# Kernel optimization log

Hardware: AMD Instinct MI355X
Metric: run time of the kernel (lower is better)

## Reference

```python
import jax, jax.numpy as jnp
import numpy as np

T, N, F_IN, H, C, E = 64, 2000, 32, 64, 10, 32000
EPS = 1e-5  # BatchNorm eps (PyG BatchNorm default)


def setup_inputs() -> dict:
    key = jax.random.key(0)
    ks = jax.random.split(key, 32)
    nrm = lambda i, shape, s=0.05: jax.random.normal(ks[i], shape, jnp.float32) * s
    return {
        "x_seq": jax.random.normal(ks[0], (T, N, F_IN), jnp.float32),
        "edge_index": jax.random.randint(ks[1], (2, E), 0, N),
        "edge_weight": jax.random.uniform(ks[2], (E,), jnp.float32),
        "causal_weight": nrm(3, (N, N), 0.01),  # torch.randn(N,N)*0.01
        "lin_in_w": nrm(4, (H, F_IN)), "lin_in_b": nrm(5, (H,)),
        "fusion_w": nrm(6, (H, 2 * H)), "fusion_b": nrm(7, (H,)),
        "gcn_w0": nrm(8, (H, H)), "gcn_b0": nrm(9, (H,)),
        "gcn_w1": nrm(10, (H, H)), "gcn_b1": nrm(11, (H,)),
        "bn0_g": jnp.ones((H,), jnp.float32), "bn0_b": jnp.zeros((H,), jnp.float32),
        "bn0_m": nrm(12, (H,)), "bn0_v": 0.5 + jax.random.uniform(ks[13], (H,), jnp.float32),
        "bn1_g": jnp.ones((H,), jnp.float32), "bn1_b": jnp.zeros((H,), jnp.float32),
        "bn1_m": nrm(14, (H,)), "bn1_v": 0.5 + jax.random.uniform(ks[15], (H,), jnp.float32),
        "gru_wih0": nrm(16, (3 * H, H)), "gru_whh0": nrm(17, (3 * H, H)),
        "gru_bih0": nrm(18, (3 * H,)), "gru_bhh0": nrm(19, (3 * H,)),
        "gru_wih1": nrm(20, (3 * H, H)), "gru_whh1": nrm(21, (3 * H, H)),
        "gru_bih1": nrm(22, (3 * H,)), "gru_bhh1": nrm(23, (3 * H,)),
        "bnout_g": jnp.ones((H,), jnp.float32), "bnout_b": jnp.zeros((H,), jnp.float32),
        "bnout_m": nrm(24, (H,)), "bnout_v": 0.5 + jax.random.uniform(ks[25], (H,), jnp.float32),
        "lin_out_w": nrm(26, (C, H)), "lin_out_b": nrm(27, (C,)),
    }


def _bn(x, g, b, m, v):
    # eval-mode BatchNorm over the feature (last) axis with running stats
    return (x - m) * jax.lax.rsqrt(v + EPS) * g + b


def _gru_layer(xs, wih, whh, bih, bhh):
    # torch nn.GRU single layer, batch_first=False: xs [T, B, H_in]
    n_batch, h = xs.shape[1], whh.shape[1]

    def step(hprev, xt):
        gi = xt @ wih.T + bih            # [B, 3H]
        gh = hprev @ whh.T + bhh         # [B, 3H]
        i_r, i_z, i_n = jnp.split(gi, 3, axis=-1)
        h_r, h_z, h_n = jnp.split(gh, 3, axis=-1)
        r = jax.nn.sigmoid(i_r + h_r)
        z = jax.nn.sigmoid(i_z + h_z)
        n = jnp.tanh(i_n + r * h_n)
        hnew = (1.0 - z) * n + z * hprev
        return hnew, hnew

    h0 = jnp.zeros((n_batch, h), xs.dtype)
    _, ys = jax.lax.scan(step, h0, xs)
    return ys


def reference(x_seq, edge_index, edge_weight, causal_weight, lin_in_w, lin_in_b,
              fusion_w, fusion_b, gcn_w0, gcn_b0, gcn_w1, gcn_b1,
              bn0_g, bn0_b, bn0_m, bn0_v, bn1_g, bn1_b, bn1_m, bn1_v,
              gru_wih0, gru_whh0, gru_bih0, gru_bhh0,
              gru_wih1, gru_whh1, gru_bih1, gru_bhh1,
              bnout_g, bnout_b, bnout_m, bnout_v, lin_out_w, lin_out_b):
    n = x_seq.shape[1]
    src, dst = edge_index[0], edge_index[1]
    loops = jnp.arange(n)
    # GCN normalization with added self-loops (PyG gcn_norm, fill_value=1)
    src_f = jnp.concatenate([src, loops])
    dst_f = jnp.concatenate([dst, loops])
    w_f = jnp.concatenate([edge_weight, jnp.ones((n,), edge_weight.dtype)])
    deg = jnp.zeros((n,), x_seq.dtype).at[dst_f].add(w_f)
    dis = jax.lax.rsqrt(jnp.maximum(deg, 1e-12))
    norm = dis[src_f] * w_f * dis[dst_f]             # [E+N]

    # per-timestep pipeline, vectorized over T (same math as the Python loop)
    x = jax.nn.relu(jnp.einsum('tnf,hf->tnh', x_seq, lin_in_w) + lin_in_b)  # [T,N,H]
    wc = jax.nn.softmax(causal_weight, axis=1)                              # [N,N]
    x_agg = jnp.einsum('ij,tjh->tih', wc, x)
    x = jax.nn.relu(jnp.concatenate([x, x_agg], axis=-1) @ fusion_w.T + fusion_b)

    def gcn(xx, w, b):
        xw = xx @ w.T                                         # [T,N,H]
        msgs = jnp.take(xw, src_f, axis=1) * norm[None, :, None]  # [T,E+N,H]
        agg = jnp.zeros_like(xw).at[:, dst_f].add(msgs)
        return agg + b

    x = jax.nn.relu(_bn(gcn(x, gcn_w0, gcn_b0), bn0_g, bn0_b, bn0_m, bn0_v))
    # dropout between GCN layers is identity in eval mode
    x = jax.nn.relu(_bn(gcn(x, gcn_w1, gcn_b1), bn1_g, bn1_b, bn1_m, bn1_v))

    h = _gru_layer(x, gru_wih0, gru_whh0, gru_bih0, gru_bhh0)
    h = _gru_layer(h, gru_wih1, gru_whh1, gru_bih1, gru_bhh1)
    h_last = jax.nn.relu(_bn(h[-1], bnout_g, bnout_b, bnout_m, bnout_v))
    out = h_last @ lin_out_w.T + lin_out_b                   # [N, C]
    return jax.nn.log_softmax(out, axis=-1)
```

## Files before the change

kernel.cpp:

```cpp
#include <hip/hip_runtime.h>
#include <hip/hip_bf16.h>
#include <math.h>

#define TT 64
#define NN 2000
#define FIN 32
#define HH 64
#define CC 10
#define EE 32000
#define ETOT 34000
#define THL 4096
#define EPSBN 1e-5f
#define NB 16

#define OFF_WC   0u
#define OFF_XA   4000000u
#define OFF_XB   12192000u
#define OFF_XC   20384000u
#define OFF_DEG  28576000u
#define OFF_H1   28578048u
#define OFF_CNT  28706048u
#define OFF_CUR  28708096u
#define OFF_OFF  28710144u
#define OFF_CSRS 28712208u
#define OFF_CSRN 28746224u
#define OFF_HST  28780240u

typedef __attribute__((ext_vector_type(8))) short short8v;
typedef __attribute__((ext_vector_type(4))) float f32x4;

__device__ __forceinline__ float fsigmoid(float x) { return 1.f / (1.f + __expf(-x)); }
__device__ __forceinline__ float ftanh(float x) {
    float e = __expf(2.f * x);
    return (e - 1.f) / (e + 1.f);
}
__device__ __forceinline__ unsigned short f2bf(float f) {
    __hip_bfloat16 h = __float2bfloat16(f);
    return *reinterpret_cast<unsigned short*>(&h);
}
__device__ __forceinline__ float bf2f(unsigned short u) {
    unsigned int x = ((unsigned int)u) << 16;
    return __int_as_float(x);
}
__device__ __forceinline__ void gload_lds16(const unsigned short* g, unsigned short* l) {
    __builtin_amdgcn_global_load_lds(
        (const __attribute__((address_space(1))) unsigned int*)g,
        (__attribute__((address_space(3))) unsigned int*)l,
        16, 0, 0);
}

__global__ void k_zero(int* cnt, int* cur, float* deg) {
    int i = blockIdx.x * 256 + threadIdx.x;
    if (i < 2048) { cnt[i] = 0; cur[i] = 0; deg[i] = 0.f; }
}

__global__ void k_count(const int* __restrict__ ei, const float* __restrict__ ew,
                        int* cnt, float* deg) {
    int e = blockIdx.x * 256 + threadIdx.x;
    if (e < ETOT) {
        int dst; float w;
        if (e < EE) { dst = ei[EE + e]; w = ew[e]; }
        else        { dst = e - EE;     w = 1.f; }
        atomicAdd(&cnt[dst], 1);
        atomicAdd(&deg[dst], w);
    }
}

__global__ __launch_bounds__(1024) void k_scan(const int* __restrict__ cnt, int* off) {
    __shared__ int s[2048];
    int tid = threadIdx.x;
    s[tid]        = (tid        < NN) ? cnt[tid]        : 0;
    s[tid + 1024] = (tid + 1024 < NN) ? cnt[tid + 1024] : 0;
    __syncthreads();
    for (int d = 1; d < 2048; d <<= 1) {
        int idx = (tid + 1) * (d << 1) - 1;
        if (idx < 2048) s[idx] += s[idx - d];
        __syncthreads();
    }
    if (tid == 0) s[2047] = 0;
    __syncthreads();
    for (int d = 1024; d >= 1; d >>= 1) {
        int idx = (tid + 1) * (d << 1) - 1;
        if (idx < 2048) { int t = s[idx - d]; s[idx - d] = s[idx]; s[idx] += t; }
        __syncthreads();
    }
    off[tid] = s[tid];
    off[tid + 1024] = s[tid + 1024];
}

__global__ void k_fill(const int* __restrict__ ei, const float* __restrict__ ew,
                       const float* __restrict__ deg, const int* __restrict__ off,
                       int* cur, int* csr_src, float* csr_nrm) {
    int e = blockIdx.x * 256 + threadIdx.x;
    if (e < ETOT) {
        int src, dst; float w;
        if (e < EE) { src = ei[e]; dst = ei[EE + e]; w = ew[e]; }
        else        { src = dst = e - EE;            w = 1.f; }
        float ds = rsqrtf(fmaxf(deg[src], 1e-12f));
        float dd = rsqrtf(fmaxf(deg[dst], 1e-12f));
        int pos = off[dst] + atomicAdd(&cur[dst], 1);
        csr_src[pos] = src;
        csr_nrm[pos] = ds * w * dd;
    }
}

__global__ __launch_bounds__(256) void k_softmax(const float* __restrict__ CW,
                                                 unsigned short* __restrict__ WCH) {
    __shared__ float row[NN];
    __shared__ float red[256];
    int r = blockIdx.x, tid = threadIdx.x;
    const float* in = CW + (size_t)r * NN;
    float mx = -1e30f;
    for (int i = tid; i < NN; i += 256) { float v = in[i]; row[i] = v; mx = fmaxf(mx, v); }
    red[tid] = mx; __syncthreads();
    for (int s = 128; s > 0; s >>= 1) {
        if (tid < s) red[tid] = fmaxf(red[tid], red[tid + s]);
        __syncthreads();
    }
    mx = red[0]; __syncthreads();
    float sm = 0.f;
    for (int i = tid; i < NN; i += 256) { float e = __expf(row[i] - mx); row[i] = e; sm += e; }
    red[tid] = sm; __syncthreads();
    for (int s = 128; s > 0; s >>= 1) {
        if (tid < s) red[tid] += red[tid + s];
        __syncthreads();
    }
    float inv = 1.f / red[0];
    unsigned short* out = WCH + (size_t)r * 2048;
    for (int i = tid; i < 2048; i += 256)
        out[i] = (i < NN) ? f2bf(row[i] * inv) : (unsigned short)0;
}

__global__ __launch_bounds__(256) void k_lin2(const float* __restrict__ XS,
                                              const float* __restrict__ W,
                                              const float* __restrict__ b,
                                              unsigned short* __restrict__ OUT) {
    __shared__ float Wt[FIN][68];
    __shared__ float As[FIN][68];
    int tid = threadIdx.x;
    int n = blockIdx.x;
    for (int i = tid; i < HH * FIN; i += 256) { int o = i >> 5, k = i & 31; Wt[k][o] = W[i]; }
    int row = tid >> 2, kq = tid & 3;
    {
        const float4* src = (const float4*)(XS + ((size_t)row * NN + n) * FIN + kq * 8);
        float4 v0 = src[0], v1 = src[1];
        As[kq * 8 + 0][row] = v0.x; As[kq * 8 + 1][row] = v0.y;
        As[kq * 8 + 2][row] = v0.z; As[kq * 8 + 3][row] = v0.w;
        As[kq * 8 + 4][row] = v1.x; As[kq * 8 + 5][row] = v1.y;
        As[kq * 8 + 6][row] = v1.z; As[kq * 8 + 7][row] = v1.w;
    }
    __syncthreads();
    int tx = tid & 15, ty = tid >> 4;
    float acc[4][4] = {};
#pragma unroll
    for (int k = 0; k < FIN; ++k) {
        float4 av = *(const float4*)&As[k][ty * 4];
        float4 wv = *(const float4*)&Wt[k][tx * 4];
        acc[0][0] += av.x * wv.x; acc[0][1] += av.x * wv.y; acc[0][2] += av.x * wv.z; acc[0][3] += av.x * wv.w;
        acc[1][0] += av.y * wv.x; acc[1][1] += av.y * wv.y; acc[1][2] += av.y * wv.z; acc[1][3] += av.y * wv.w;
        acc[2][0] += av.z * wv.x; acc[2][1] += av.z * wv.y; acc[2][2] += av.z * wv.z; acc[2][3] += av.z * wv.w;
        acc[3][0] += av.w * wv.x; acc[3][1] += av.w * wv.y; acc[3][2] += av.w * wv.z; acc[3][3] += av.w * wv.w;
    }
    float4 bv = *(const float4*)(b + tx * 4);
#pragma unroll
    for (int ii = 0; ii < 4; ++ii) {
        float o0 = fmaxf(acc[ii][0] + bv.x, 0.f);
        float o1 = fmaxf(acc[ii][1] + bv.y, 0.f);
        float o2 = fmaxf(acc[ii][2] + bv.z, 0.f);
        float o3 = fmaxf(acc[ii][3] + bv.w, 0.f);
        unsigned int p0 = (unsigned int)f2bf(o0) | ((unsigned int)f2bf(o1) << 16);
        unsigned int p1 = (unsigned int)f2bf(o2) | ((unsigned int)f2bf(o3) << 16);
        uint2 pk; pk.x = p0; pk.y = p1;
        *(uint2*)(OUT + ((size_t)n * TT + ty * 4 + ii) * HH + tx * 4) = pk;
    }
}

__global__ __launch_bounds__(256) void k_tr(const unsigned short* __restrict__ X,
                                            unsigned short* __restrict__ XT) {
    __shared__ unsigned short tile[64][65];
    int cb = blockIdx.x * 64;
    int kb = blockIdx.y * 64;
    int tid = threadIdx.x;
    int r = tid >> 2, cq = tid & 3;
    unsigned short vals[16];
    if (kb + r < NN) {
        const uint4* src = (const uint4*)(X + (size_t)(kb + r) * THL + cb + cq * 16);
        uint4 u0 = src[0], u1 = src[1];
        *(uint4*)vals = u0; *(uint4*)(vals + 8) = u1;
    } else {
#pragma unroll
        for (int j = 0; j < 16; ++j) vals[j] = 0;
    }
#pragma unroll
    for (int j = 0; j < 16; ++j) tile[cq * 16 + j][r] = vals[j];
    __syncthreads();
    int cl = tid >> 2, kq = tid & 3;
    unsigned short tmp[16];
#pragma unroll
    for (int j = 0; j < 16; ++j) tmp[j] = tile[cl][kq * 16 + j];
    unsigned short* dst = XT + (size_t)(cb + cl) * 2048 + kb + kq * 16;
    *(uint4*)dst = *(uint4*)tmp;
    *(uint4*)(dst + 8) = *(uint4*)(tmp + 8);
}

__global__ __launch_bounds__(256, 1) void k_gemm_bf(const unsigned short* __restrict__ A,
                                                    const unsigned short* __restrict__ B,
                                                    unsigned short* __restrict__ CH) {
    __shared__ unsigned short As[128][64];
    __shared__ unsigned short Bs[128][64];
    int tid = threadIdx.x;
    int mb = blockIdx.y * 128, nb = blockIdx.x * 128;
    int w = tid >> 6, lane = tid & 63;
    int wr = w >> 1, wc = w & 1;
    int l15 = lane & 15, l4 = lane >> 4;
    f32x4 acc[4][4] = {};
    int r_base = w * 8 + (lane >> 3);
    int colu = (lane & 7) * 8;
    for (int kt = 0; kt < 32; ++kt) {
        __syncthreads();
#pragma unroll
        for (int c = 0; c < 4; ++c) {
            int row = c * 32 + r_base;
            gload_lds16(A + (size_t)(mb + row) * 2048 + kt * 64 + colu, &As[c * 32 + w * 8][0]);
            gload_lds16(B + (size_t)(nb + row) * 2048 + kt * 64 + colu, &Bs[c * 32 + w * 8][0]);
        }
        __syncthreads();
#pragma unroll
        for (int kk = 0; kk < 2; ++kk) {
            short8v af[4], bfr[4];
#pragma unroll
            for (int f = 0; f < 4; ++f) {
                af[f]  = *(const short8v*)&As[wr * 64 + f * 16 + l15][kk * 32 + l4 * 8];
                bfr[f] = *(const short8v*)&Bs[wc * 64 + f * 16 + l15][kk * 32 + l4 * 8];
            }
#pragma unroll
            for (int fm = 0; fm < 4; ++fm)
#pragma unroll
                for (int fn = 0; fn < 4; ++fn)
                    acc[fm][fn] = __builtin_amdgcn_mfma_f32_16x16x32_bf16(af[fm], bfr[fn], acc[fm][fn], 0, 0, 0);
        }
    }
    unsigned short* epi = (unsigned short*)(&As[0][0]) + (size_t)w * (16 * 72);
    int erow8 = lane >> 3;
    int ecol8 = lane & 7;
#pragma unroll
    for (int fm = 0; fm < 4; ++fm) {
        __syncthreads();
#pragma unroll
        for (int fn = 0; fn < 4; ++fn)
#pragma unroll
            for (int rr = 0; rr < 4; ++rr)
                epi[(l4 * 4 + rr) * 72 + fn * 16 + l15] = f2bf(acc[fm][fn][rr]);
        __syncthreads();
#pragma unroll
        for (int rh = 0; rh < 2; ++rh) {
            int lrow = rh * 8 + erow8;
            int grow = mb + wr * 64 + fm * 16 + lrow;
            if (grow < NN) {
                *(uint4*)(CH + (size_t)grow * THL + nb + wc * 64 + ecol8 * 8)
                    = *(const uint4*)&epi[lrow * 72 + ecol8 * 8];
            }
        }
    }
}

__global__ __launch_bounds__(256) void k_fusxw(const unsigned short* __restrict__ X,
                                               const unsigned short* __restrict__ XAH,
                                               const float* __restrict__ W,
                                               const float* __restrict__ b,
                                               const float* __restrict__ W0,
                                               unsigned short* __restrict__ OUT) {
    __shared__ float Wt[2 * HH][68];
    __shared__ float As[HH][68];
    int tid = threadIdx.x;
    size_t r0 = (size_t)blockIdx.x * 64;
    for (int i = tid; i < HH * 2 * HH; i += 256) { int o = i >> 7, k = i & 127; Wt[k][o] = W[i]; }
    int row = tid >> 2, kq = tid & 3;
    int tx = tid & 15, ty = tid >> 4;
    float acc[4][4] = {};
    __syncthreads();
    {
        const uint4* s = (const uint4*)(X + (r0 + row) * HH + kq * 16);
        uint4 u0 = s[0], u1 = s[1];
        unsigned short us[16];
        *(uint4*)us = u0; *(uint4*)(us + 8) = u1;
#pragma unroll
        for (int j = 0; j < 16; ++j)
            As[kq * 16 + j][row] = bf2f(us[j]);
    }
    __syncthreads();
#pragma unroll
    for (int k = 0; k < HH; ++k) {
        float4 av = *(const float4*)&As[k][ty * 4];
        float4 wv = *(const float4*)&Wt[k][tx * 4];
        acc[0][0] += av.x * wv.x; acc[0][1] += av.x * wv.y; acc[0][2] += av.x * wv.z; acc[0][3] += av.x * wv.w;
        acc[1][0] += av.y * wv.x; acc[1][1] += av.y * wv.y; acc[1][2] += av.y * wv.z; acc[1][3] += av.y * wv.w;
        acc[2][0] += av.z * wv.x; acc[2][1] += av.z * wv.y; acc[2][2] += av.z * wv.z; acc[2][3] += av.z * wv.w;
        acc[3][0] += av.w * wv.x; acc[3][1] += av.w * wv.y; acc[3][2] += av.w * wv.z; acc[3][3] += av.w * wv.w;
    }
    __syncthreads();
    {
        const uint4* s = (const uint4*)(XAH + (r0 + row) * HH + kq * 16);
        uint4 u0 = s[0], u1 = s[1];
        unsigned short us[16];
        *(uint4*)us = u0; *(uint4*)(us + 8) = u1;
#pragma unroll
        for (int j = 0; j < 16; ++j)
            As[kq * 16 + j][row] = bf2f(us[j]);
    }
    __syncthreads();
#pragma unroll
    for (int k = 0; k < HH; ++k) {
        float4 av = *(const float4*)&As[k][ty * 4];
        float4 wv = *(const float4*)&Wt[HH + k][tx * 4];
        acc[0][0] += av.x * wv.x; acc[0][1] += av.x * wv.y; acc[0][2] += av.x * wv.z; acc[0][3] += av.x * wv.w;
        acc[1][0] += av.y * wv.x; acc[1][1] += av.y * wv.y; acc[1][2] += av.y * wv.z; acc[1][3] += av.y * wv.w;
        acc[2][0] += av.z * wv.x; acc[2][1] += av.z * wv.y; acc[2][2] += av.z * wv.z; acc[2][3] += av.z * wv.w;
        acc[3][0] += av.w * wv.x; acc[3][1] += av.w * wv.y; acc[3][2] += av.w * wv.z; acc[3][3] += av.w * wv.w;
    }
    float4 bv = *(const float4*)(b + tx * 4);
    __syncthreads();
#pragma unroll
    for (int ii = 0; ii < 4; ++ii) {
        As[tx * 4 + 0][ty * 4 + ii] = fmaxf(acc[ii][0] + bv.x, 0.f);
        As[tx * 4 + 1][ty * 4 + ii] = fmaxf(acc[ii][1] + bv.y, 0.f);
        As[tx * 4 + 2][ty * 4 + ii] = fmaxf(acc[ii][2] + bv.z, 0.f);
        As[tx * 4 + 3][ty * 4 + ii] = fmaxf(acc[ii][3] + bv.w, 0.f);
    }
    for (int i = tid; i < HH * HH; i += 256) { int o = i >> 6, k = i & 63; Wt[k][o] = W0[i]; }
    __syncthreads();
    float a2[4][4] = {};
#pragma unroll
    for (int k = 0; k < HH; ++k) {
        float4 av = *(const float4*)&As[k][ty * 4];
        float4 wv = *(const float4*)&Wt[k][tx * 4];
        a2[0][0] += av.x * wv.x; a2[0][1] += av.x * wv.y; a2[0][2] += av.x * wv.z; a2[0][3] += av.x * wv.w;
        a2[1][0] += av.y * wv.x; a2[1][1] += av.y * wv.y; a2[1][2] += av.y * wv.z; a2[1][3] += av.y * wv.w;
        a2[2][0] += av.z * wv.x; a2[2][1] += av.z * wv.y; a2[2][2] += av.z * wv.z; a2[2][3] += av.z * wv.w;
        a2[3][0] += av.w * wv.x; a2[3][1] += av.w * wv.y; a2[3][2] += av.w * wv.z; a2[3][3] += av.w * wv.w;
    }
#pragma unroll
    for (int ii = 0; ii < 4; ++ii) {
        unsigned int p0 = (unsigned int)f2bf(a2[ii][0]) | ((unsigned int)f2bf(a2[ii][1]) << 16);
        unsigned int p1 = (unsigned int)f2bf(a2[ii][2]) | ((unsigned int)f2bf(a2[ii][3]) << 16);
        uint2 pk; pk.x = p0; pk.y = p1;
        *(uint2*)(OUT + (r0 + ty * 4 + ii) * HH + tx * 4) = pk;
    }
}

__global__ __launch_bounds__(256) void k_aggxw(const unsigned short* __restrict__ XW,
                                               const int* __restrict__ off,
                                               const int* __restrict__ csr_src,
                                               const float* __restrict__ csr_nrm,
                                               const float* __restrict__ bias,
                                               const float* __restrict__ g,
                                               const float* __restrict__ bb,
                                               const float* __restrict__ m,
                                               const float* __restrict__ v,
                                               const float* __restrict__ W1,
                                               unsigned short* __restrict__ OUT) {
    __shared__ float Rs[HH][18];
    __shared__ float Wt[HH][68];
    int dst = blockIdx.x, ch = blockIdx.y, tid = threadIdx.x;
    int base = ch * 1024 + tid * 4;
    for (int i = tid; i < HH * HH; i += 256) { int o = i >> 6, k = i & 63; Wt[k][o] = W1[i]; }
    float4 acc = make_float4(0.f, 0.f, 0.f, 0.f);
    int beg = off[dst], end = off[dst + 1];
    for (int e = beg; e < end; ++e) {
        int src = csr_src[e];
        float w = csr_nrm[e];
        uint2 u = *(const uint2*)(XW + (size_t)src * THL + base);
        acc.x += w * bf2f((unsigned short)(u.x & 0xffff));
        acc.y += w * bf2f((unsigned short)(u.x >> 16));
        acc.z += w * bf2f((unsigned short)(u.y & 0xffff));
        acc.w += w * bf2f((unsigned short)(u.y >> 16));
    }
    int h0 = base & 63;
    int rloc = tid >> 4;
    float4 bs = *(const float4*)(bias + h0);
    float4 gv = *(const float4*)(g + h0);
    float4 vv = *(const float4*)(v + h0);
    float4 mv = *(const float4*)(m + h0);
    float4 bv = *(const float4*)(bb + h0);
    Rs[h0 + 0][rloc] = fmaxf((acc.x + bs.x - mv.x) * rsqrtf(vv.x + EPSBN) * gv.x + bv.x, 0.f);
    Rs[h0 + 1][rloc] = fmaxf((acc.y + bs.y - mv.y) * rsqrtf(vv.y + EPSBN) * gv.y + bv.y, 0.f);
    Rs[h0 + 2][rloc] = fmaxf((acc.z + bs.z - mv.z) * rsqrtf(vv.z + EPSBN) * gv.z + bv.z, 0.f);
    Rs[h0 + 3][rloc] = fmaxf((acc.w + bs.w - mv.w) * rsqrtf(vv.w + EPSBN) * gv.w + bv.w, 0.f);
    __syncthreads();
    int c4 = tid & 15;
    float a2[4] = {0.f, 0.f, 0.f, 0.f};
#pragma unroll
    for (int k = 0; k < HH; ++k) {
        float a = Rs[k][rloc];
        float4 wv = *(const float4*)&Wt[k][c4 * 4];
        a2[0] += a * wv.x; a2[1] += a * wv.y; a2[2] += a * wv.z; a2[3] += a * wv.w;
    }
    size_t grow = (size_t)dst * TT + ch * 16 + rloc;
    unsigned int p0 = (unsigned int)f2bf(a2[0]) | ((unsigned int)f2bf(a2[1]) << 16);
    unsigned int p1 = (unsigned int)f2bf(a2[2]) | ((unsigned int)f2bf(a2[3]) << 16);
    uint2 pk; pk.x = p0; pk.y = p1;
    *(uint2*)(OUT + grow * HH + c4 * 4) = pk;
}

__global__ __launch_bounds__(256) void k_agg(const unsigned short* __restrict__ XW,
                                             const int* __restrict__ off,
                                             const int* __restrict__ csr_src,
                                             const float* __restrict__ csr_nrm,
                                             const float* __restrict__ bias,
                                             const float* __restrict__ g,
                                             const float* __restrict__ bb,
                                             const float* __restrict__ m,
                                             const float* __restrict__ v,
                                             unsigned short* __restrict__ OUT) {
    int dst = blockIdx.x, ch = blockIdx.y, tid = threadIdx.x;
    int base = ch * 1024 + tid * 4;
    float4 acc = make_float4(0.f, 0.f, 0.f, 0.f);
    int beg = off[dst], end = off[dst + 1];
    for (int e = beg; e < end; ++e) {
        int src = csr_src[e];
        float w = csr_nrm[e];
        uint2 u = *(const uint2*)(XW + (size_t)src * THL + base);
        acc.x += w * bf2f((unsigned short)(u.x & 0xffff));
        acc.y += w * bf2f((unsigned short)(u.x >> 16));
        acc.z += w * bf2f((unsigned short)(u.y & 0xffff));
        acc.w += w * bf2f((unsigned short)(u.y >> 16));
    }
    int h0 = base & 63;
    float4 bs = *(const float4*)(bias + h0);
    float4 gv = *(const float4*)(g + h0);
    float4 vv = *(const float4*)(v + h0);
    float4 mv = *(const float4*)(m + h0);
    float4 bv = *(const float4*)(bb + h0);
    float o0 = fmaxf((acc.x + bs.x - mv.x) * rsqrtf(vv.x + EPSBN) * gv.x + bv.x, 0.f);
    float o1 = fmaxf((acc.y + bs.y - mv.y) * rsqrtf(vv.y + EPSBN) * gv.y + bv.y, 0.f);
    float o2 = fmaxf((acc.z + bs.z - mv.z) * rsqrtf(vv.z + EPSBN) * gv.z + bv.z, 0.f);
    float o3 = fmaxf((acc.w + bs.w - mv.w) * rsqrtf(vv.w + EPSBN) * gv.w + bv.w, 0.f);
    unsigned int p0 = (unsigned int)f2bf(o0) | ((unsigned int)f2bf(o1) << 16);
    unsigned int p1 = (unsigned int)f2bf(o2) | ((unsigned int)f2bf(o3) << 16);
    uint2 pk; pk.x = p0; pk.y = p1;
    *(uint2*)(OUT + (size_t)dst * THL + base) = pk;
}

__global__ __launch_bounds__(256, 1) void k_gruM(const unsigned short* __restrict__ IN,
                                                 const float* __restrict__ wih0, const float* __restrict__ whh0,
                                                 const float* __restrict__ bih0, const float* __restrict__ bhh0,
                                                 const float* __restrict__ wih1, const float* __restrict__ whh1,
                                                 const float* __restrict__ bih1, const float* __restrict__ bhh1,
                                                 float* __restrict__ hout) {
    __shared__ float hf0[NB][68];
    __shared__ float hf1[NB][68];
    __shared__ unsigned short hb0[NB][72];
    __shared__ unsigned short hb1[NB][72];
    int tid = threadIdx.x;
    int w = tid >> 6, lane = tid & 63;
    int l15 = lane & 15, l4 = lane >> 4;
    int nb0 = blockIdx.x * NB;
    short8v bw[4][3][2];
    const float* Wm[4] = { wih0, whh0, wih1, whh1 };
#pragma unroll
    for (int m = 0; m < 4; ++m)
#pragma unroll
        for (int g = 0; g < 3; ++g)
#pragma unroll
            for (int kk = 0; kk < 2; ++kk) {
                const float* src = Wm[m] + (size_t)(64 * g + 16 * w + l15) * HH + kk * 32 + l4 * 8;
                float4 v0 = *(const float4*)src;
                float4 v1 = *(const float4*)(src + 4);
                short8v f;
                f[0] = (short)f2bf(v0.x); f[1] = (short)f2bf(v0.y);
                f[2] = (short)f2bf(v0.z); f[3] = (short)f2bf(v0.w);
                f[4] = (short)f2bf(v1.x); f[5] = (short)f2bf(v1.y);
                f[6] = (short)f2bf(v1.z); f[7] = (short)f2bf(v1.w);
                bw[m][g][kk] = f;
            }
    int jr = 16 * w + l15;
    float b0r = bih0[jr] + bhh0[jr];
    float b0z = bih0[64 + jr] + bhh0[64 + jr];
    float b0n = bih0[128 + jr];
    float h0n = bhh0[128 + jr];
    float b1r = bih1[jr] + bhh1[jr];
    float b1z = bih1[64 + jr] + bhh1[64 + jr];
    float b1n = bih1[128 + jr];
    float h1n = bhh1[128 + jr];
    for (int i = tid; i < NB * 68; i += 256) { ((float*)hf0)[i] = 0.f; ((float*)hf1)[i] = 0.f; }
    for (int i = tid; i < NB * 72; i += 256) { ((unsigned short*)hb0)[i] = 0; ((unsigned short*)hb1)[i] = 0; }
    __syncthreads();
    const unsigned short* xb = IN + (size_t)(nb0 + l15) * (TT * HH);
    uint4 xu[2];
    xu[0] = *(const uint4*)(xb + l4 * 8);
    xu[1] = *(const uint4*)(xb + 32 + l4 * 8);
#pragma unroll 1
    for (int t = 0; t <= TT; ++t) {
        bool act0 = (t < TT);
        bool act1 = (t >= 1);
        short8v ax[2], ah0[2], ah1[2];
        ax[0] = *(const short8v*)&xu[0];
        ax[1] = *(const short8v*)&xu[1];
#pragma unroll
        for (int kk = 0; kk < 2; ++kk) {
            ah0[kk] = *(const short8v*)&hb0[l15][kk * 32 + l4 * 8];
            ah1[kk] = *(const short8v*)&hb1[l15][kk * 32 + l4 * 8];
        }
        __syncthreads();
        if (t + 1 < TT) {
            const unsigned short* xs = xb + (size_t)(t + 1) * HH;
            xu[0] = *(const uint4*)(xs + l4 * 8);
            xu[1] = *(const uint4*)(xs + 32 + l4 * 8);
        }
        if (act0) {
            f32x4 gr = { b0r, b0r, b0r, b0r };
            f32x4 gz = { b0z, b0z, b0z, b0z };
            f32x4 gn = { b0n, b0n, b0n, b0n };
            f32x4 hr = { 0.f, 0.f, 0.f, 0.f };
            f32x4 hz = { 0.f, 0.f, 0.f, 0.f };
            f32x4 hn = { h0n, h0n, h0n, h0n };
#pragma unroll
            for (int kk = 0; kk < 2; ++kk) {
                gr = __builtin_amdgcn_mfma_f32_16x16x32_bf16(ax[kk], bw[0][0][kk], gr, 0, 0, 0);
                gz = __builtin_amdgcn_mfma_f32_16x16x32_bf16(ax[kk], bw[0][1][kk], gz, 0, 0, 0);
                gn = __builtin_amdgcn_mfma_f32_16x16x32_bf16(ax[kk], bw[0][2][kk], gn, 0, 0, 0);
                hr = __builtin_amdgcn_mfma_f32_16x16x32_bf16(ah0[kk], bw[1][0][kk], hr, 0, 0, 0);
                hz = __builtin_amdgcn_mfma_f32_16x16x32_bf16(ah0[kk], bw[1][1][kk], hz, 0, 0, 0);
                hn = __builtin_amdgcn_mfma_f32_16x16x32_bf16(ah0[kk], bw[1][2][kk], hn, 0, 0, 0);
            }
#pragma unroll
            for (int i = 0; i < 4; ++i) {
                int node = l4 * 4 + i;
                float r = fsigmoid(gr[i] + hr[i]);
                float z = fsigmoid(gz[i] + hz[i]);
                float nn2 = ftanh(gn[i] + r * hn[i]);
                float ho = hf0[node][jr];
                float hv = (1.f - z) * nn2 + z * ho;
                hf0[node][jr] = hv;
                hb0[node][jr] = f2bf(hv);
            }
        }
        if (act1) {
            f32x4 gr = { b1r, b1r, b1r, b1r };
            f32x4 gz = { b1z, b1z, b1z, b1z };
            f32x4 gn = { b1n, b1n, b1n, b1n };
            f32x4 hr = { 0.f, 0.f, 0.f, 0.f };
            f32x4 hz = { 0.f, 0.f, 0.f, 0.f };
            f32x4 hn = { h1n, h1n, h1n, h1n };
#pragma unroll
            for (int kk = 0; kk < 2; ++kk) {
                gr = __builtin_amdgcn_mfma_f32_16x16x32_bf16(ah0[kk], bw[2][0][kk], gr, 0, 0, 0);
                gz = __builtin_amdgcn_mfma_f32_16x16x32_bf16(ah0[kk], bw[2][1][kk], gz, 0, 0, 0);
                gn = __builtin_amdgcn_mfma_f32_16x16x32_bf16(ah0[kk], bw[2][2][kk], gn, 0, 0, 0);
                hr = __builtin_amdgcn_mfma_f32_16x16x32_bf16(ah1[kk], bw[3][0][kk], hr, 0, 0, 0);
                hz = __builtin_amdgcn_mfma_f32_16x16x32_bf16(ah1[kk], bw[3][1][kk], hz, 0, 0, 0);
                hn = __builtin_amdgcn_mfma_f32_16x16x32_bf16(ah1[kk], bw[3][2][kk], hn, 0, 0, 0);
            }
#pragma unroll
            for (int i = 0; i < 4; ++i) {
                int node = l4 * 4 + i;
                float r = fsigmoid(gr[i] + hr[i]);
                float z = fsigmoid(gz[i] + hz[i]);
                float nn2 = ftanh(gn[i] + r * hn[i]);
                float ho = hf1[node][jr];
                float hv = (1.f - z) * nn2 + z * ho;
                hf1[node][jr] = hv;
                hb1[node][jr] = f2bf(hv);
            }
        }
        __syncthreads();
    }
    for (int i = tid; i < NB * HH; i += 256) {
        int node = i >> 6, j = i & 63;
        hout[(size_t)(nb0 + node) * HH + j] = hf1[node][j];
    }
}

__global__ __launch_bounds__(256) void k_head(const float* __restrict__ Hf,
                                              const float* __restrict__ g, const float* __restrict__ b,
                                              const float* __restrict__ m, const float* __restrict__ v,
                                              const float* __restrict__ W, const float* __restrict__ wb,
                                              float* __restrict__ out) {
    __shared__ float hb[4][HH];
    __shared__ float lg[4][CC];
    int tid = threadIdx.x;
    int n0 = blockIdx.x * 4;
    int wv = tid >> 6, lane = tid & 63;
    int n = n0 + wv;
    float x = Hf[(size_t)n * HH + lane];
    x = (x - m[lane]) * rsqrtf(v[lane] + EPSBN) * g[lane] + b[lane];
    hb[wv][lane] = fmaxf(x, 0.f);
    __syncthreads();
    if (tid < 4 * CC) {
        int nn = tid / CC, c = tid % CC;
        float acc = wb[c];
        for (int f = 0; f < HH; ++f) acc += hb[nn][f] * W[c * HH + f];
        lg[nn][c] = acc;
    }
    __syncthreads();
    if (tid < 4 * CC) {
        int nn = tid / CC, c = tid % CC;
        float mx = -1e30f;
#pragma unroll
        for (int i = 0; i < CC; ++i) mx = fmaxf(mx, lg[nn][i]);
        float s = 0.f;
#pragma unroll
        for (int i = 0; i < CC; ++i) s += __expf(lg[nn][i] - mx);
        out[(size_t)(n0 + nn) * CC + c] = lg[nn][c] - mx - __logf(s);
    }
}

extern "C" void kernel_launch(void* const* d_in, const int* in_sizes, int n_in,
                              void* d_out, int out_size, void* d_ws, size_t ws_size,
                              hipStream_t stream) {
    const float* x_seq     = (const float*)d_in[0];
    const int*   edge_idx  = (const int*)d_in[1];
    const float* edge_w    = (const float*)d_in[2];
    const float* causal_w  = (const float*)d_in[3];
    const float* lin_in_w  = (const float*)d_in[4];
    const float* lin_in_b  = (const float*)d_in[5];
    const float* fusion_w  = (const float*)d_in[6];
    const float* fusion_b  = (const float*)d_in[7];
    const float* gcn_w0    = (const float*)d_in[8];
    const float* gcn_b0    = (const float*)d_in[9];
    const float* gcn_w1    = (const float*)d_in[10];
    const float* gcn_b1    = (const float*)d_in[11];
    const float* bn0_g = (const float*)d_in[12], *bn0_b = (const float*)d_in[13];
    const float* bn0_m = (const float*)d_in[14], *bn0_v = (const float*)d_in[15];
    const float* bn1_g = (const float*)d_in[16], *bn1_b = (const float*)d_in[17];
    const float* bn1_m = (const float*)d_in[18], *bn1_v = (const float*)d_in[19];
    const float* wih0 = (const float*)d_in[20], *whh0 = (const float*)d_in[21];
    const float* bih0 = (const float*)d_in[22], *bhh0 = (const float*)d_in[23];
    const float* wih1 = (const float*)d_in[24], *whh1 = (const float*)d_in[25];
    const float* bih1 = (const float*)d_in[26], *bhh1 = (const float*)d_in[27];
    const float* bno_g = (const float*)d_in[28], *bno_b = (const float*)d_in[29];
    const float* bno_m = (const float*)d_in[30], *bno_v = (const float*)d_in[31];
    const float* lout_w = (const float*)d_in[32], *lout_b = (const float*)d_in[33];
    float* out = (float*)d_out;

    float* wsf = (float*)d_ws;
    unsigned short* WCH = (unsigned short*)(wsf + OFF_WC);
    unsigned short* XLH = (unsigned short*)(wsf + OFF_XA);
    unsigned short* XAT = (unsigned short*)(wsf + OFF_XC);
    unsigned short* XBH = (unsigned short*)(wsf + OFF_XB);
    unsigned short* XW1 = (unsigned short*)(wsf + OFF_XA);
    unsigned short* XCH = (unsigned short*)(wsf + OFF_XC);
    float* DEG = wsf + OFF_DEG;
    int* CNT   = (int*)(wsf + OFF_CNT);
    int* CUR   = (int*)(wsf + OFF_CUR);
    int* OFFP  = (int*)(wsf + OFF_OFF);
    int* CSRS  = (int*)(wsf + OFF_CSRS);
    float* CSRN = wsf + OFF_CSRN;
    float* HST  = wsf + OFF_HST;

    k_zero<<<8, 256, 0, stream>>>(CNT, CUR, DEG);
    k_count<<<(ETOT + 255) / 256, 256, 0, stream>>>(edge_idx, edge_w, CNT, DEG);
    k_scan<<<1, 1024, 0, stream>>>(CNT, OFFP);
    k_fill<<<(ETOT + 255) / 256, 256, 0, stream>>>(edge_idx, edge_w, DEG, OFFP, CUR, CSRS, CSRN);

    hipMemsetAsync(WCH, 0, (size_t)2048 * 2048 * 2, stream);
    k_softmax<<<NN, 256, 0, stream>>>(causal_w, WCH);
    k_lin2<<<NN, 256, 0, stream>>>(x_seq, lin_in_w, lin_in_b, XLH);
    dim3 tg(THL / 64, 2048 / 64);
    k_tr<<<tg, 256, 0, stream>>>(XLH, XAT);
    dim3 gg(THL / 128, 2048 / 128);
    k_gemm_bf<<<gg, 256, 0, stream>>>(WCH, XAT, XBH);
    k_fusxw<<<NN, 256, 0, stream>>>(XLH, XBH, fusion_w, fusion_b, gcn_w0, XBH);
    dim3 ag(NN, 4);
    k_aggxw<<<ag, 256, 0, stream>>>(XBH, OFFP, CSRS, CSRN, gcn_b0, bn0_g, bn0_b, bn0_m, bn0_v,
                                    gcn_w1, XW1);
    k_agg<<<ag, 256, 0, stream>>>(XW1, OFFP, CSRS, CSRN, gcn_b1, bn1_g, bn1_b, bn1_m, bn1_v, XCH);

    k_gruM<<<NN / NB, 256, 0, stream>>>(XCH, wih0, whh0, bih0, bhh0,
                                        wih1, whh1, bih1, bhh1, HST);

    k_head<<<NN / 4, 256, 0, stream>>>(HST, bno_g, bno_b, bno_m, bno_v, lout_w, lout_b, out);
}
```

Baseline: 350.6 us.

## Split GRU layers across separate waves and fold WCH memset into softmax

The fused two-layer GRU kernel now runs 512 threads per block. Waves 0-3 compute layer 0 and waves 4-7 compute layer 1 concurrently in the wavefront-skewed pipeline, rather than each wave doing both layers serially. Each wave now holds half the weight fragments, and the fp32 hidden state stays in registers instead of shared memory. Separately, the full-buffer memset of the padded softmax matrix is dropped: extra softmax blocks zero the padding rows, and the existing loop already zeros the padding columns. This removes one launch and a redundant write pass.

```diff
diff --git a/kernel.cpp b/kernel.cpp
--- a/kernel.cpp
+++ b/kernel.cpp
@@ -106,9 +106,15 @@
 
 __global__ __launch_bounds__(256) void k_softmax(const float* __restrict__ CW,
                                                  unsigned short* __restrict__ WCH) {
+    int r = blockIdx.x, tid = threadIdx.x;
+    unsigned short* out = WCH + (size_t)r * 2048;
+    if (r >= NN) {
+        uint2 z; z.x = 0u; z.y = 0u;
+        for (int i = tid; i < 512; i += 256) ((uint2*)out)[i] = z;
+        return;
+    }
     __shared__ float row[NN];
     __shared__ float red[256];
-    int r = blockIdx.x, tid = threadIdx.x;
     const float* in = CW + (size_t)r * NN;
     float mx = -1e30f;
     for (int i = tid; i < NN; i += 256) { float v = in[i]; row[i] = v; mx = fmaxf(mx, v); }
@@ -126,7 +132,6 @@
         __syncthreads();
     }
     float inv = 1.f / red[0];
-    unsigned short* out = WCH + (size_t)r * 2048;
     for (int i = tid; i < 2048; i += 256)
         out[i] = (i < NN) ? f2bf(row[i] * inv) : (unsigned short)0;
 }
@@ -441,133 +446,122 @@
     *(uint2*)(OUT + (size_t)dst * THL + base) = pk;
 }
 
-__global__ __launch_bounds__(256, 1) void k_gruM(const unsigned short* __restrict__ IN,
+__global__ __launch_bounds__(512, 1) void k_gruM(const unsigned short* __restrict__ IN,
                                                  const float* __restrict__ wih0, const float* __restrict__ whh0,
                                                  const float* __restrict__ bih0, const float* __restrict__ bhh0,
                                                  const float* __restrict__ wih1, const float* __restrict__ whh1,
                                                  const float* __restrict__ bih1, const float* __restrict__ bhh1,
                                                  float* __restrict__ hout) {
-    __shared__ float hf0[NB][68];
-    __shared__ float hf1[NB][68];
     __shared__ unsigned short hb0[NB][72];
     __shared__ unsigned short hb1[NB][72];
     int tid = threadIdx.x;
     int w = tid >> 6, lane = tid & 63;
     int l15 = lane & 15, l4 = lane >> 4;
     int nb0 = blockIdx.x * NB;
-    short8v bw[4][3][2];
-    const float* Wm[4] = { wih0, whh0, wih1, whh1 };
-#pragma unroll
-    for (int m = 0; m < 4; ++m)
-#pragma unroll
-        for (int g = 0; g < 3; ++g)
-#pragma unroll
-            for (int kk = 0; kk < 2; ++kk) {
-                const float* src = Wm[m] + (size_t)(64 * g + 16 * w + l15) * HH + kk * 32 + l4 * 8;
-                float4 v0 = *(const float4*)src;
-                float4 v1 = *(const float4*)(src + 4);
-                short8v f;
-                f[0] = (short)f2bf(v0.x); f[1] = (short)f2bf(v0.y);
-                f[2] = (short)f2bf(v0.z); f[3] = (short)f2bf(v0.w);
-                f[4] = (short)f2bf(v1.x); f[5] = (short)f2bf(v1.y);
-                f[6] = (short)f2bf(v1.z); f[7] = (short)f2bf(v1.w);
-                bw[m][g][kk] = f;
-            }
-    int jr = 16 * w + l15;
-    float b0r = bih0[jr] + bhh0[jr];
-    float b0z = bih0[64 + jr] + bhh0[64 + jr];
-    float b0n = bih0[128 + jr];
-    float h0n = bhh0[128 + jr];
-    float b1r = bih1[jr] + bhh1[jr];
-    float b1z = bih1[64 + jr] + bhh1[64 + jr];
-    float b1n = bih1[128 + jr];
-    float h1n = bhh1[128 + jr];
-    for (int i = tid; i < NB * 68; i += 256) { ((float*)hf0)[i] = 0.f; ((float*)hf1)[i] = 0.f; }
-    for (int i = tid; i < NB * 72; i += 256) { ((unsigned short*)hb0)[i] = 0; ((unsigned short*)hb1)[i] = 0; }
+    bool isL0 = (w < 4);
+    int cg = isL0 ? w : (w - 4);
+    int jr = 16 * cg + l15;
+    const float* Wx = isL0 ? wih0 : wih1;
+    const float* Wh = isL0 ? whh0 : whh1;
+    short8v bwx[3][2], bwh[3][2];
+#pragma unroll
+    for (int g = 0; g < 3; ++g)
+#pragma unroll
+        for (int kk = 0; kk < 2; ++kk) {
+            const float* sx = Wx + (size_t)(64 * g + jr) * HH + kk * 32 + l4 * 8;
+            float4 x0 = *(const float4*)sx;
+            float4 x1 = *(const float4*)(sx + 4);
+            short8v fx;
+            fx[0] = (short)f2bf(x0.x); fx[1] = (short)f2bf(x0.y);
+            fx[2] = (short)f2bf(x0.z); fx[3] = (short)f2bf(x0.w);
+            fx[4] = (short)f2bf(x1.x); fx[5] = (short)f2bf(x1.y);
+            fx[6] = (short)f2bf(x1.z); fx[7] = (short)f2bf(x1.w);
+            bwx[g][kk] = fx;
+            const float* sh = Wh + (size_t)(64 * g + jr) * HH + kk * 32 + l4 * 8;
+            float4 h0v = *(const float4*)sh;
+            float4 h1v = *(const float4*)(sh + 4);
+            short8v fh;
+            fh[0] = (short)f2bf(h0v.x); fh[1] = (short)f2bf(h0v.y);
+            fh[2] = (short)f2bf(h0v.z); fh[3] = (short)f2bf(h0v.w);
+            fh[4] = (short)f2bf(h1v.x); fh[5] = (short)f2bf(h1v.y);
+            fh[6] = (short)f2bf(h1v.z); fh[7] = (short)f2bf(h1v.w);
+            bwh[g][kk] = fh;
+        }
+    const float* bi = isL0 ? bih0 : bih1;
+    const float* bh = isL0 ? bhh0 : bhh1;
+    float br  = bi[jr] + bh[jr];
+    float bz  = bi[64 + jr] + bh[64 + jr];
+    float bn  = bi[128 + jr];
+    float hnb = bh[128 + jr];
+    float rh[4] = {0.f, 0.f, 0.f, 0.f};
+    for (int i = tid; i < NB * 72; i += 512) {
+        ((unsigned short*)hb0)[i] = 0;
+        ((unsigned short*)hb1)[i] = 0;
+    }
     __syncthreads();
     const unsigned short* xb = IN + (size_t)(nb0 + l15) * (TT * HH);
-    uint4 xu[2];
-    xu[0] = *(const uint4*)(xb + l4 * 8);
-    xu[1] = *(const uint4*)(xb + 32 + l4 * 8);
+    uint4 xu0, xu1;
+    if (isL0) {
+        xu0 = *(const uint4*)(xb + l4 * 8);
+        xu1 = *(const uint4*)(xb + 32 + l4 * 8);
+    }
 #pragma unroll 1
     for (int t = 0; t <= TT; ++t) {
-        bool act0 = (t < TT);
-        bool act1 = (t >= 1);
-        short8v ax[2], ah0[2], ah1[2];
-        ax[0] = *(const short8v*)&xu[0];
-        ax[1] = *(const short8v*)&xu[1];
-#pragma unroll
-        for (int kk = 0; kk < 2; ++kk) {
-            ah0[kk] = *(const short8v*)&hb0[l15][kk * 32 + l4 * 8];
-            ah1[kk] = *(const short8v*)&hb1[l15][kk * 32 + l4 * 8];
-        }
-        __syncthreads();
-        if (t + 1 < TT) {
+        bool act = isL0 ? (t < TT) : (t >= 1);
+        short8v aA[2], aB[2];
+        if (isL0) {
+            aA[0] = *(const short8v*)&xu0;
+            aA[1] = *(const short8v*)&xu1;
+            aB[0] = *(const short8v*)&hb0[l15][l4 * 8];
+            aB[1] = *(const short8v*)&hb0[l15][32 + l4 * 8];
+        } else {
+            aA[0] = *(const short8v*)&hb0[l15][l4 * 8];
+            aA[1] = *(const short8v*)&hb0[l15][32 + l4 * 8];
+            aB[0] = *(const short8v*)&hb1[l15][l4 * 8];
+            aB[1] = *(const short8v*)&hb1[l15][32 + l4 * 8];
+        }
+        __syncthreads();
+        if (isL0 && t + 1 < TT) {
             const unsigned short* xs = xb + (size_t)(t + 1) * HH;
-            xu[0] = *(const uint4*)(xs + l4 * 8);
-            xu[1] = *(const uint4*)(xs + 32 + l4 * 8);
-        }
-        if (act0) {
-            f32x4 gr = { b0r, b0r, b0r, b0r };
-            f32x4 gz = { b0z, b0z, b0z, b0z };
-            f32x4 gn = { b0n, b0n, b0n, b0n };
+            xu0 = *(const uint4*)(xs + l4 * 8);
+            xu1 = *(const uint4*)(xs + 32 + l4 * 8);
+        }
+        if (act) {
+            f32x4 gr = { br, br, br, br };
+            f32x4 gz = { bz, bz, bz, bz };
+            f32x4 gn = { bn, bn, bn, bn };
             f32x4 hr = { 0.f, 0.f, 0.f, 0.f };
             f32x4 hz = { 0.f, 0.f, 0.f, 0.f };
-            f32x4 hn = { h0n, h0n, h0n, h0n };
+            f32x4 hn = { hnb, hnb, hnb, hnb };
 #pragma unroll
             for (int kk = 0; kk < 2; ++kk) {
-                gr = __builtin_amdgcn_mfma_f32_16x16x32_bf16(ax[kk], bw[0][0][kk], gr, 0, 0, 0);
-                gz = __builtin_amdgcn_mfma_f32_16x16x32_bf16(ax[kk], bw[0][1][kk], gz, 0, 0, 0);
-                gn = __builtin_amdgcn_mfma_f32_16x16x32_bf16(ax[kk], bw[0][2][kk], gn, 0, 0, 0);
-                hr = __builtin_amdgcn_mfma_f32_16x16x32_bf16(ah0[kk], bw[1][0][kk], hr, 0, 0, 0);
-                hz = __builtin_amdgcn_mfma_f32_16x16x32_bf16(ah0[kk], bw[1][1][kk], hz, 0, 0, 0);
-                hn = __builtin_amdgcn_mfma_f32_16x16x32_bf16(ah0[kk], bw[1][2][kk], hn, 0, 0, 0);
+                gr = __builtin_amdgcn_mfma_f32_16x16x32_bf16(aA[kk], bwx[0][kk], gr, 0, 0, 0);
+                gz = __builtin_amdgcn_mfma_f32_16x16x32_bf16(aA[kk], bwx[1][kk], gz, 0, 0, 0);
+                gn = __builtin_amdgcn_mfma_f32_16x16x32_bf16(aA[kk], bwx[2][kk], gn, 0, 0, 0);
+                hr = __builtin_amdgcn_mfma_f32_16x16x32_bf16(aB[kk], bwh[0][kk], hr, 0, 0, 0);
+                hz = __builtin_amdgcn_mfma_f32_16x16x32_bf16(aB[kk], bwh[1][kk], hz, 0, 0, 0);
+                hn = __builtin_amdgcn_mfma_f32_16x16x32_bf16(aB[kk], bwh[2][kk], hn, 0, 0, 0);
             }
+            unsigned short* hbw = isL0 ? &hb0[0][0] : &hb1[0][0];
 #pragma unroll
             for (int i = 0; i < 4; ++i) {
                 int node = l4 * 4 + i;
                 float r = fsigmoid(gr[i] + hr[i]);
                 float z = fsigmoid(gz[i] + hz[i]);
                 float nn2 = ftanh(gn[i] + r * hn[i]);
-                float ho = hf0[node][jr];
-                float hv = (1.f - z) * nn2 + z * ho;
-                hf0[node][jr] = hv;
-                hb0[node][jr] = f2bf(hv);
+                float hv = (1.f - z) * nn2 + z * rh[i];
+                rh[i] = hv;
+                hbw[node * 72 + jr] = f2bf(hv);
             }
         }
-        if (act1) {
-            f32x4 gr = { b1r, b1r, b1r, b1r };
-            f32x4 gz = { b1z, b1z, b1z, b1z };
-            f32x4 gn = { b1n, b1n, b1n, b1n };
-            f32x4 hr = { 0.f, 0.f, 0.f, 0.f };
-            f32x4 hz = { 0.f, 0.f, 0.f, 0.f };
-            f32x4 hn = { h1n, h1n, h1n, h1n };
-#pragma unroll
-            for (int kk = 0; kk < 2; ++kk) {
-                gr = __builtin_amdgcn_mfma_f32_16x16x32_bf16(ah0[kk], bw[2][0][kk], gr, 0, 0, 0);
-                gz = __builtin_amdgcn_mfma_f32_16x16x32_bf16(ah0[kk], bw[2][1][kk], gz, 0, 0, 0);
-                gn = __builtin_amdgcn_mfma_f32_16x16x32_bf16(ah0[kk], bw[2][2][kk], gn, 0, 0, 0);
-                hr = __builtin_amdgcn_mfma_f32_16x16x32_bf16(ah1[kk], bw[3][0][kk], hr, 0, 0, 0);
-                hz = __builtin_amdgcn_mfma_f32_16x16x32_bf16(ah1[kk], bw[3][1][kk], hz, 0, 0, 0);
-                hn = __builtin_amdgcn_mfma_f32_16x16x32_bf16(ah1[kk], bw[3][2][kk], hn, 0, 0, 0);
-            }
-#pragma unroll
-            for (int i = 0; i < 4; ++i) {
-                int node = l4 * 4 + i;
-                float r = fsigmoid(gr[i] + hr[i]);
-                float z = fsigmoid(gz[i] + hz[i]);
-                float nn2 = ftanh(gn[i] + r * hn[i]);
-                float ho = hf1[node][jr];
-                float hv = (1.f - z) * nn2 + z * ho;
-                hf1[node][jr] = hv;
-                hb1[node][jr] = f2bf(hv);
-            }
-        }
-        __syncthreads();
-    }
-    for (int i = tid; i < NB * HH; i += 256) {
-        int node = i >> 6, j = i & 63;
-        hout[(size_t)(nb0 + node) * HH + j] = hf1[node][j];
+        __syncthreads();
+    }
+    if (!isL0) {
+#pragma unroll
+        for (int i = 0; i < 4; ++i) {
+            int node = l4 * 4 + i;
+            hout[(size_t)(nb0 + node) * HH + jr] = rh[i];
+        }
     }
 }
 
@@ -653,8 +647,7 @@
     k_scan<<<1, 1024, 0, stream>>>(CNT, OFFP);
     k_fill<<<(ETOT + 255) / 256, 256, 0, stream>>>(edge_idx, edge_w, DEG, OFFP, CUR, CSRS, CSRN);
 
-    hipMemsetAsync(WCH, 0, (size_t)2048 * 2048 * 2, stream);
-    k_softmax<<<NN, 256, 0, stream>>>(causal_w, WCH);
+    k_softmax<<<2048, 256, 0, stream>>>(causal_w, WCH);
     k_lin2<<<NN, 256, 0, stream>>>(x_seq, lin_in_w, lin_in_b, XLH);
     dim3 tg(THL / 64, 2048 / 64);
     k_tr<<<tg, 256, 0, stream>>>(XLH, XAT);
@@ -666,7 +659,7 @@
                                     gcn_w1, XW1);
     k_agg<<<ag, 256, 0, stream>>>(XW1, OFFP, CSRS, CSRN, gcn_b1, bn1_g, bn1_b, bn1_m, bn1_v, XCH);
 
-    k_gruM<<<NN / NB, 256, 0, stream>>>(XCH, wih0, whh0, bih0, bhh0,
+    k_gruM<<<NN / NB, 512, 0, stream>>>(XCH, wih0, whh0, bih0, bhh0,
                                         wih1, whh1, bih1, bhh1, HST);
 
     k_head<<<NN / 4, 256, 0, stream>>>(HST, bno_g, bno_b, bno_m, bno_v, lout_w, lout_b, out);
```

Result: faster. 329.2 us (median of 2 runs) (-6.1%).
